# Optimization experiments

Hardware: AMD Instinct MI355X
Metric: run time of the kernel (lower is better)

The kernel has to match this reference:

```python
import jax, jax.numpy as jnp
import numpy as np

B, T, C = 2, 2048, 1024
N_HEAD = 16
HEAD_DIM = C // N_HEAD  # 64


def _apply_rope(x, inv_freq):
    # x: [B, H, T, hd]. Matches the torch module's mixed RoPE variant:
    # cos/sin built from cat(freqs, freqs) but x split by even/odd strides.
    Tn, hd = x.shape[2], x.shape[3]
    t = jnp.arange(Tn, dtype=inv_freq.dtype)
    freqs = t[:, None] * inv_freq[None, :]            # [T, hd/2]
    emb = jnp.concatenate([freqs, freqs], axis=-1)    # [T, hd]
    cos = jnp.cos(emb)[None, None, :, :]
    sin = jnp.sin(emb)[None, None, :, :]
    x1 = x[..., 0::2]
    x2 = x[..., 1::2]
    # interleave (-x2, x1) back to last dim: stack then flatten last two dims
    x_rot = jnp.stack((-x2, x1), axis=-1).reshape(x.shape)
    return x * cos + x_rot * sin


def setup_inputs() -> dict:
    key = jax.random.key(0)
    k1, k2, k3 = jax.random.split(key, 3)
    x = jax.random.normal(k1, (B, T, C), dtype=jnp.float32)
    w_qkv = jax.random.normal(k2, (C, 3 * C), dtype=jnp.float32) * 0.02
    w_proj = jax.random.normal(k3, (C, C), dtype=jnp.float32) * 0.02
    return {"x": x, "w_qkv": w_qkv, "w_proj": w_proj}


def reference(x, w_qkv, w_proj):
    Bn, Tn, Cn = x.shape
    hd = HEAD_DIM
    inv_freq = 1.0 / (10000.0 ** (jnp.arange(0, hd, 2, dtype=jnp.float32) / hd))

    qkv = jnp.einsum('btc,cd->btd', x, w_qkv)  # [B, T, 3C]
    q, k, v = jnp.split(qkv, 3, axis=2)
    # [B, T, C] -> [B, H, T, hd]
    q = q.reshape(Bn, Tn, N_HEAD, hd).transpose(0, 2, 1, 3)
    k = k.reshape(Bn, Tn, N_HEAD, hd).transpose(0, 2, 1, 3)
    v = v.reshape(Bn, Tn, N_HEAD, hd).transpose(0, 2, 1, 3)

    q = _apply_rope(q, inv_freq)
    k = _apply_rope(k, inv_freq)

    scale = 1.0 / jnp.sqrt(jnp.asarray(hd, dtype=q.dtype))
    scores = jnp.einsum('bhqd,bhkd->bhqk', q, k) * scale  # [B, H, T, T]
    causal = jnp.tril(jnp.ones((Tn, Tn), dtype=bool))
    scores = jnp.where(causal[None, None, :, :], scores, -jnp.inf)
    attn = jax.nn.softmax(scores, axis=-1)
    out = jnp.einsum('bhqk,bhkd->bhqd', attn, v)          # [B, H, T, hd]
    y = out.transpose(0, 2, 1, 3).reshape(Bn, Tn, Cn)     # [B, T, C]
    return jnp.einsum('btc,cd->btd', y, w_proj)
```

## Files before the change

### kernel.cpp

```cpp
#include <hip/hip_runtime.h>
#include <hip/hip_bf16.h>

typedef unsigned short u16;
typedef unsigned int u32;
typedef __attribute__((ext_vector_type(8))) __bf16 bf16x8;
typedef __attribute__((ext_vector_type(4))) float f32x4;
typedef __attribute__((ext_vector_type(4))) u16 u16x4;
typedef __attribute__((ext_vector_type(4))) u32 u32x4;

__device__ __forceinline__ u16 f2bf(float f) {
  return __builtin_bit_cast(u16, (__bf16)f);
}
__device__ __forceinline__ float bf2f(u16 h) {
  return __builtin_bit_cast(float, (u32)h << 16);
}

__device__ __forceinline__ void gload_lds16(const void* g, void* l) {
  __builtin_amdgcn_global_load_lds((const __attribute__((address_space(1))) void*)g,
                                   (__attribute__((address_space(3))) void*)l, 16, 0, 0);
}

__global__ __launch_bounds__(256) void cvt_kernel(const float* __restrict__ in, u16* __restrict__ out) {
  const int i = (blockIdx.x * 256 + threadIdx.x) * 4;
  const float4 v = *(const float4*)(in + i);
  u16x4 r = {f2bf(v.x), f2bf(v.y), f2bf(v.z), f2bf(v.w)};
  *(u16x4*)(out + i) = r;
}

__global__ __launch_bounds__(256) void transpose_w(const float* __restrict__ w, u16* __restrict__ wt,
                                                   int K, int N) {
  __shared__ u16 tile[64][65];
  const int n0 = blockIdx.x * 64, k0 = blockIdx.y * 64;
  const int tid = threadIdx.x;
#pragma unroll
  for (int it = 0; it < 16; ++it) {
    const int idx = it * 256 + tid;
    const int r = idx >> 6, c = idx & 63;
    tile[r][c] = f2bf(w[(size_t)(k0 + r) * N + n0 + c]);
  }
  __syncthreads();
#pragma unroll
  for (int it = 0; it < 16; ++it) {
    const int idx = it * 256 + tid;
    const int r2 = idx >> 6, c2 = idx & 63;
    wt[(size_t)(n0 + r2) * K + k0 + c2] = tile[c2][r2];
  }
}

template <int OUT_F32>
__global__ __launch_bounds__(256) void gemm_bt(const u16* __restrict__ A, const u16* __restrict__ Bt,
                                               void* __restrict__ Cout, int M, int N, int K) {
  __shared__ u16 As[2][128 * 32];
  __shared__ u16 Bs[2][128 * 32];
  const int tid = threadIdx.x;
  const int wave = tid >> 6;
  const int lane = tid & 63;
  const int la = lane & 15, lb = lane >> 4;
  const int nwg = gridDim.x * gridDim.y;
  int lid = blockIdx.y * gridDim.x + blockIdx.x;
  lid = (lid & 7) * (nwg >> 3) + (lid >> 3);
  const int m0 = (lid % gridDim.x) * 128, n0 = (lid / gridDim.x) * 128;
  const int wr = (wave >> 1) * 64, wc = (wave & 1) * 64;
  const int srow = lane >> 2;
  const int scol = (lane & 3) * 8;
  const int c0 = wave * 2;

  auto stage = [&](int bb, int k0) {
#pragma unroll
    for (int c2 = 0; c2 < 2; ++c2) {
      const int c = c0 + c2;
      const int row = c * 16 + srow;
      gload_lds16(A + (size_t)(m0 + row) * K + k0 + scol, As[bb] + c * 512);
      gload_lds16(Bt + (size_t)(n0 + row) * K + k0 + scol, Bs[bb] + c * 512);
    }
  };

  f32x4 acc[4][4] = {};
  const int nk = K >> 5;
  stage(0, 0);
  __syncthreads();
  int cur = 0;
  for (int t = 0; t < nk; ++t) {
    if (t + 1 < nk) stage(cur ^ 1, (t + 1) * 32);
    bf16x8 af[4], bfr[4];
#pragma unroll
    for (int m = 0; m < 4; ++m) af[m] = *(const bf16x8*)&As[cur][(wr + m * 16 + la) * 32 + lb * 8];
#pragma unroll
    for (int n = 0; n < 4; ++n) bfr[n] = *(const bf16x8*)&Bs[cur][(wc + n * 16 + la) * 32 + lb * 8];
#pragma unroll
    for (int m = 0; m < 4; ++m)
#pragma unroll
      for (int n = 0; n < 4; ++n)
        acc[m][n] = __builtin_amdgcn_mfma_f32_16x16x32_bf16(af[m], bfr[n], acc[m][n], 0, 0, 0);
    __syncthreads();
    cur ^= 1;
  }
#pragma unroll
  for (int m = 0; m < 4; ++m)
#pragma unroll
    for (int n = 0; n < 4; ++n)
#pragma unroll
      for (int j = 0; j < 4; ++j) {
        const int row = m0 + wr + m * 16 + lb * 4 + j;
        const int col = n0 + wc + n * 16 + la;
        if (OUT_F32)
          ((float*)Cout)[(size_t)row * N + col] = acc[m][n][j];
        else
          ((u16*)Cout)[(size_t)row * N + col] = f2bf(acc[m][n][j]);
      }
}

__global__ __launch_bounds__(256) void rope_kernel(const u16* __restrict__ QKV, u16* __restrict__ Q,
                                                   u16* __restrict__ K, u16* __restrict__ Vt) {
  const int tt = blockIdx.x * 64;
  const int bh = blockIdx.y;
  const int b = bh >> 4, h = bh & 15;
  const int tid = threadIdx.x;
  __shared__ u16 vtile[64][65];
  const float NEG = -0.41524101186f;
  const float QSC = 0.18033688011f;

  const int i = tid & 31;
  const int d0 = 2 * i;
  const int j0 = d0 & 31, j1 = (d0 + 1) & 31;
  const float invf0 = exp2f(NEG * (float)j0);
  const float invf1 = exp2f(NEG * (float)j1);
  const int tl0 = tid >> 5;
  float s0, c0v, s1, c1v, sd0, cd0, sd1, cd1;
  sincosf((float)(tt + tl0) * invf0, &s0, &c0v);
  sincosf((float)(tt + tl0) * invf1, &s1, &c1v);
  sincosf(8.0f * invf0, &sd0, &cd0);
  sincosf(8.0f * invf1, &sd1, &cd1);

#pragma unroll
  for (int it = 0; it < 8; ++it) {
    const int t = tt + tl0 + it * 8;
    const size_t base = ((size_t)(b * 2048 + t)) * 3072 + h * 64 + d0;
    const size_t ob = ((size_t)bh * 2048 + t) * 64 + d0;
    {
      const float x0 = bf2f(QKV[base]), x1 = bf2f(QKV[base + 1]);
      const u32 lo = f2bf((x0 * c0v - x1 * s0) * QSC);
      const u32 hi = f2bf((x1 * c1v + x0 * s1) * QSC);
      *(u32*)(Q + ob) = lo | (hi << 16);
    }
    {
      const float x0 = bf2f(QKV[base + 1024]), x1 = bf2f(QKV[base + 1025]);
      const u32 lo = f2bf(x0 * c0v - x1 * s0);
      const u32 hi = f2bf(x1 * c1v + x0 * s1);
      *(u32*)(K + ob) = lo | (hi << 16);
    }
    const float nc0 = c0v * cd0 - s0 * sd0, ns0 = s0 * cd0 + c0v * sd0;
    c0v = nc0; s0 = ns0;
    const float nc1 = c1v * cd1 - s1 * sd1, ns1 = s1 * cd1 + c1v * sd1;
    c1v = nc1; s1 = ns1;
  }
#pragma unroll
  for (int it = 0; it < 8; ++it) {
    const int idx = it * 256 + tid;
    const int tl = idx >> 5, dd = (idx & 31) * 2;
    const size_t base = ((size_t)(b * 2048 + tt + tl)) * 3072 + 2048 + h * 64 + dd;
    vtile[tl][dd] = QKV[base];
    vtile[tl][dd + 1] = QKV[base + 1];
  }
  __syncthreads();
#pragma unroll
  for (int it = 0; it < 8; ++it) {
    const int idx = it * 256 + tid;
    const int dl = idx >> 5, tp = (idx & 31) * 2;
    const u32 val = (u32)vtile[tp][dl] | ((u32)vtile[tp + 1][dl] << 16);
    *(u32*)(Vt + ((size_t)bh * 64 + dl) * 2048 + tt + tp) = val;
  }
}

__global__ __launch_bounds__(256) void attn_kernel(const u16* __restrict__ Q, const u16* __restrict__ K,
                                                   const u16* __restrict__ Vt, u16* __restrict__ Y) {
  const int L = blockIdx.y * 16 + blockIdx.x;
  const int xcd = L & 7, slot = L >> 3;
  const int bh = xcd * 4 + (slot & 3);
  const int B0 = slot >> 2;
  const int b = bh >> 4, h = bh & 15;
  const int wave = threadIdx.x >> 6, lane = threadIdx.x & 63;
  const int la = lane & 15, lb = lane >> 4;
  const int NT = 32 - B0;
  const int ktE0 = B0 + 1;
  const int q0s[2] = {B0 * 64 + wave * 16, (31 - B0) * 64 + wave * 16};

  __shared__ __align__(16) u16 KV[2][2][4096];

  const size_t plane = (size_t)bh * (2048 * 64);
  const char* Kb = (const char*)(K + plane);
  const char* Vb = (const char*)(Vt + plane);

  auto stage = [&](int buf, int kt) {
#pragma unroll
    for (int it = 0; it < 2; ++it) {
      const int ci = it * 256 + wave * 64 + lane;
      const int row = ci >> 3;
      const int cbs = ((ci & 7) * 16) ^ ((row & 7) << 4);
      const int n2 = row >> 4, rho = row & 15;
      const int srow = ((n2 & 1) << 5) + ((rho >> 2) << 3) + ((n2 >> 1) << 2) + (rho & 3);
      gload_lds16(Kb + (size_t)(kt * 64 + srow) * 128 + cbs,
                  (char*)&KV[buf][0][0] + it * 4096 + wave * 1024);
      gload_lds16(Vb + (size_t)row * 4096 + (size_t)kt * 128 + cbs,
                  (char*)&KV[buf][1][0] + it * 4096 + wave * 1024);
    }
  };

  stage(0, 0);

  bf16x8 qf[2][2];
#pragma unroll
  for (int st = 0; st < 2; ++st)
#pragma unroll
    for (int s = 0; s < 2; ++s)
      qf[st][s] = *(const bf16x8*)(Q + plane + (size_t)(q0s[st] + la) * 64 + s * 32 + lb * 8);

  f32x4 o[2][4] = {};
  float mreg[2] = {-1.0e30f, -1.0e30f};
  float plr[2] = {0.f, 0.f};

  const int x0 = (la & 7) << 4;
  const int cu0 = ((lb * 16) ^ x0) >> 1;
  const int cu1 = ((64 + lb * 16) ^ x0) >> 1;

  __syncthreads();
  int buf = 0;
  for (int kt = 0; kt < NT; ++kt) {
    if (kt + 1 < NT) stage(buf ^ 1, kt + 1);
    const u16* Kc = KV[buf][0];
    const u16* Vc = KV[buf][1];

    bf16x8 kf[2][4];
#pragma unroll
    for (int n = 0; n < 4; ++n) {
      kf[0][n] = *(const bf16x8*)&Kc[(n * 16 + la) * 64 + cu0];
      kf[1][n] = *(const bf16x8*)&Kc[(n * 16 + la) * 64 + cu1];
    }

    bf16x8 paf[2][2];

#pragma unroll
    for (int st = 0; st < 2; ++st) {
      if (st == 0 && kt >= ktE0) continue;
      const int q0 = q0s[st];
      const int rowq = q0 + la;
      f32x4 sa[4] = {};
      __builtin_amdgcn_s_setprio(1);
#pragma unroll
      for (int s = 0; s < 2; ++s)
#pragma unroll
        for (int n = 0; n < 4; ++n)
          sa[n] = __builtin_amdgcn_mfma_f32_16x16x32_bf16(kf[s][n], qf[st][s], sa[n], 0, 0, 0);
      __builtin_amdgcn_s_setprio(0);
      if (kt * 64 + 63 > q0) {
#pragma unroll
        for (int n = 0; n < 4; ++n)
#pragma unroll
          for (int j = 0; j < 4; ++j) {
            const int col = kt * 64 + ((n & 1) << 5) + (lb << 3) + ((n >> 1) << 2) + j;
            if (col > rowq) sa[n][j] = -1.0e30f;
          }
      }
      float lmax = -1.0e30f;
#pragma unroll
      for (int n = 0; n < 4; ++n)
#pragma unroll
        for (int j = 0; j < 4; ++j) lmax = fmaxf(lmax, sa[n][j]);
      if (__any(lmax > mreg[st] + 8.0f)) {
        float v = fmaxf(lmax, __shfl_xor(lmax, 16));
        v = fmaxf(v, __shfl_xor(v, 32));
        const float mn = fmaxf(mreg[st], v);
        const float al = __builtin_amdgcn_exp2f(mreg[st] - mn);
        plr[st] *= al;
        mreg[st] = mn;
        float alj[4];
#pragma unroll
        for (int j = 0; j < 4; ++j) alj[j] = __shfl(al, lb * 4 + j);
#pragma unroll
        for (int n = 0; n < 4; ++n)
#pragma unroll
          for (int j = 0; j < 4; ++j) o[st][n][j] *= alj[j];
      }
      u32 w[4][2];
      float ps = 0.f;
#pragma unroll
      for (int n = 0; n < 4; ++n) {
        const float p0 = __builtin_amdgcn_exp2f(sa[n][0] - mreg[st]);
        const float p1 = __builtin_amdgcn_exp2f(sa[n][1] - mreg[st]);
        const float p2 = __builtin_amdgcn_exp2f(sa[n][2] - mreg[st]);
        const float p3 = __builtin_amdgcn_exp2f(sa[n][3] - mreg[st]);
        ps += (p0 + p1) + (p2 + p3);
        w[n][0] = (u32)f2bf(p0) | ((u32)f2bf(p1) << 16);
        w[n][1] = (u32)f2bf(p2) | ((u32)f2bf(p3) << 16);
      }
      plr[st] += ps;
      paf[st][0] = __builtin_bit_cast(bf16x8, (u32x4){w[0][0], w[0][1], w[2][0], w[2][1]});
      paf[st][1] = __builtin_bit_cast(bf16x8, (u32x4){w[1][0], w[1][1], w[3][0], w[3][1]});
    }

    bf16x8 vf[2][4];
#pragma unroll
    for (int n = 0; n < 4; ++n) {
      vf[0][n] = *(const bf16x8*)&Vc[(n * 16 + la) * 64 + cu0];
      vf[1][n] = *(const bf16x8*)&Vc[(n * 16 + la) * 64 + cu1];
    }
#pragma unroll
    for (int st = 0; st < 2; ++st) {
      if (st == 0 && kt >= ktE0) continue;
      __builtin_amdgcn_s_setprio(1);
#pragma unroll
      for (int n = 0; n < 4; ++n)
#pragma unroll
        for (int s = 0; s < 2; ++s)
          o[st][n] = __builtin_amdgcn_mfma_f32_16x16x32_bf16(paf[st][s], vf[s][n], o[st][n], 0, 0, 0);
      __builtin_amdgcn_s_setprio(0);
    }

    __syncthreads();
    buf ^= 1;
  }

#pragma unroll
  for (int st = 0; st < 2; ++st) {
    float ls = plr[st];
    ls += __shfl_xor(ls, 16);
    ls += __shfl_xor(ls, 32);
    const float rinv = __builtin_amdgcn_rcpf(ls);
    float rj[4];
#pragma unroll
    for (int j = 0; j < 4; ++j) rj[j] = __shfl(rinv, lb * 4 + j);
#pragma unroll
    for (int n = 0; n < 4; ++n)
#pragma unroll
      for (int j = 0; j < 4; ++j) {
        const int t = q0s[st] + lb * 4 + j;
        const int c = h * 64 + n * 16 + la;
        Y[((size_t)b * 2048 + t) * 1024 + c] = f2bf(o[st][n][j] * rj[j]);
      }
  }
}

extern "C" void kernel_launch(void* const* d_in, const int* in_sizes, int n_in, void* d_out,
                              int out_size, void* d_ws, size_t ws_size, hipStream_t stream) {
  (void)in_sizes; (void)n_in; (void)out_size; (void)ws_size;
  const float* x = (const float*)d_in[0];
  const float* w_qkv = (const float*)d_in[1];
  const float* w_proj = (const float*)d_in[2];
  char* ws = (char*)d_ws;
  u16* xb     = (u16*)(ws);
  u16* wqkvT  = (u16*)(ws + 8388608);
  u16* wprojT = (u16*)(ws + 14680064);
  u16* qkv    = (u16*)(ws + 16777216);
  u16* q      = (u16*)(ws + 41943040);
  u16* k      = (u16*)(ws + 50331648);
  u16* vt     = (u16*)(ws + 58720256);
  u16* y      = xb;

  cvt_kernel<<<dim3(4096), dim3(256), 0, stream>>>(x, xb);
  transpose_w<<<dim3(48, 16), dim3(256), 0, stream>>>(w_qkv, wqkvT, 1024, 3072);
  transpose_w<<<dim3(16, 16), dim3(256), 0, stream>>>(w_proj, wprojT, 1024, 1024);
  gemm_bt<0><<<dim3(32, 24), dim3(256), 0, stream>>>(xb, wqkvT, (void*)qkv, 4096, 3072, 1024);
  rope_kernel<<<dim3(32, 32), dim3(256), 0, stream>>>(qkv, q, k, vt);
  attn_kernel<<<dim3(16, 32), dim3(256), 0, stream>>>(q, k, vt, y);
  gemm_bt<1><<<dim3(32, 8), dim3(256), 0, stream>>>(y, wprojT, d_out, 4096, 1024, 1024);
}
```

Before: 119.9 us.

## Split paired causal query tiles into one tile per block, largest first

The attention kernel previously had each block handle two query tiles, B0 and 31-B0, which shared K/V staging and balanced causal work per block. Now each block handles a single 64-row query tile, the grid doubles to 1024 blocks, and the heaviest tiles are scheduled first so the GPU's queue balances the load. This cuts registers per thread and raises parallelism, which may improve occupancy. In exchange, K/V tiles are staged from memory about twice as often in total, since tiles are no longer shared between two query tiles.

```diff
diff --git a/kernel.cpp b/kernel.cpp
--- a/kernel.cpp
+++ b/kernel.cpp
@@ -174,16 +174,15 @@
 
 __global__ __launch_bounds__(256) void attn_kernel(const u16* __restrict__ Q, const u16* __restrict__ K,
                                                    const u16* __restrict__ Vt, u16* __restrict__ Y) {
-  const int L = blockIdx.y * 16 + blockIdx.x;
+  const int L = blockIdx.y * 32 + blockIdx.x;
   const int xcd = L & 7, slot = L >> 3;
   const int bh = xcd * 4 + (slot & 3);
-  const int B0 = slot >> 2;
+  const int beta = 31 - (slot >> 2);
   const int b = bh >> 4, h = bh & 15;
   const int wave = threadIdx.x >> 6, lane = threadIdx.x & 63;
   const int la = lane & 15, lb = lane >> 4;
-  const int NT = 32 - B0;
-  const int ktE0 = B0 + 1;
-  const int q0s[2] = {B0 * 64 + wave * 16, (31 - B0) * 64 + wave * 16};
+  const int q0 = beta * 64 + wave * 16;
+  const int NT = beta + 1;
 
   __shared__ __align__(16) u16 KV[2][2][4096];
 
@@ -208,16 +207,14 @@
 
   stage(0, 0);
 
-  bf16x8 qf[2][2];
-#pragma unroll
-  for (int st = 0; st < 2; ++st)
-#pragma unroll
-    for (int s = 0; s < 2; ++s)
-      qf[st][s] = *(const bf16x8*)(Q + plane + (size_t)(q0s[st] + la) * 64 + s * 32 + lb * 8);
-
-  f32x4 o[2][4] = {};
-  float mreg[2] = {-1.0e30f, -1.0e30f};
-  float plr[2] = {0.f, 0.f};
+  bf16x8 qf[2];
+#pragma unroll
+  for (int s = 0; s < 2; ++s)
+    qf[s] = *(const bf16x8*)(Q + plane + (size_t)(q0 + la) * 64 + s * 32 + lb * 8);
+
+  f32x4 o[4] = {};
+  float mreg = -1.0e30f;
+  float plr = 0.f;
 
   const int x0 = (la & 7) << 4;
   const int cu0 = ((lb * 16) ^ x0) >> 1;
@@ -237,66 +234,60 @@
       kf[1][n] = *(const bf16x8*)&Kc[(n * 16 + la) * 64 + cu1];
     }
 
-    bf16x8 paf[2][2];
-
-#pragma unroll
-    for (int st = 0; st < 2; ++st) {
-      if (st == 0 && kt >= ktE0) continue;
-      const int q0 = q0s[st];
-      const int rowq = q0 + la;
-      f32x4 sa[4] = {};
-      __builtin_amdgcn_s_setprio(1);
-#pragma unroll
-      for (int s = 0; s < 2; ++s)
-#pragma unroll
-        for (int n = 0; n < 4; ++n)
-          sa[n] = __builtin_amdgcn_mfma_f32_16x16x32_bf16(kf[s][n], qf[st][s], sa[n], 0, 0, 0);
-      __builtin_amdgcn_s_setprio(0);
-      if (kt * 64 + 63 > q0) {
-#pragma unroll
-        for (int n = 0; n < 4; ++n)
-#pragma unroll
-          for (int j = 0; j < 4; ++j) {
-            const int col = kt * 64 + ((n & 1) << 5) + (lb << 3) + ((n >> 1) << 2) + j;
-            if (col > rowq) sa[n][j] = -1.0e30f;
-          }
-      }
-      float lmax = -1.0e30f;
+    const int rowq = q0 + la;
+    f32x4 sa[4] = {};
+    __builtin_amdgcn_s_setprio(1);
+#pragma unroll
+    for (int s = 0; s < 2; ++s)
 #pragma unroll
       for (int n = 0; n < 4; ++n)
-#pragma unroll
-        for (int j = 0; j < 4; ++j) lmax = fmaxf(lmax, sa[n][j]);
-      if (__any(lmax > mreg[st] + 8.0f)) {
-        float v = fmaxf(lmax, __shfl_xor(lmax, 16));
-        v = fmaxf(v, __shfl_xor(v, 32));
-        const float mn = fmaxf(mreg[st], v);
-        const float al = __builtin_amdgcn_exp2f(mreg[st] - mn);
-        plr[st] *= al;
-        mreg[st] = mn;
-        float alj[4];
-#pragma unroll
-        for (int j = 0; j < 4; ++j) alj[j] = __shfl(al, lb * 4 + j);
-#pragma unroll
-        for (int n = 0; n < 4; ++n)
-#pragma unroll
-          for (int j = 0; j < 4; ++j) o[st][n][j] *= alj[j];
-      }
-      u32 w[4][2];
-      float ps = 0.f;
-#pragma unroll
-      for (int n = 0; n < 4; ++n) {
-        const float p0 = __builtin_amdgcn_exp2f(sa[n][0] - mreg[st]);
-        const float p1 = __builtin_amdgcn_exp2f(sa[n][1] - mreg[st]);
-        const float p2 = __builtin_amdgcn_exp2f(sa[n][2] - mreg[st]);
-        const float p3 = __builtin_amdgcn_exp2f(sa[n][3] - mreg[st]);
-        ps += (p0 + p1) + (p2 + p3);
-        w[n][0] = (u32)f2bf(p0) | ((u32)f2bf(p1) << 16);
-        w[n][1] = (u32)f2bf(p2) | ((u32)f2bf(p3) << 16);
-      }
-      plr[st] += ps;
-      paf[st][0] = __builtin_bit_cast(bf16x8, (u32x4){w[0][0], w[0][1], w[2][0], w[2][1]});
-      paf[st][1] = __builtin_bit_cast(bf16x8, (u32x4){w[1][0], w[1][1], w[3][0], w[3][1]});
-    }
+        sa[n] = __builtin_amdgcn_mfma_f32_16x16x32_bf16(kf[s][n], qf[s], sa[n], 0, 0, 0);
+    __builtin_amdgcn_s_setprio(0);
+    if (kt == NT - 1) {
+#pragma unroll
+      for (int n = 0; n < 4; ++n)
+#pragma unroll
+        for (int j = 0; j < 4; ++j) {
+          const int col = kt * 64 + ((n & 1) << 5) + (lb << 3) + ((n >> 1) << 2) + j;
+          if (col > rowq) sa[n][j] = -1.0e30f;
+        }
+    }
+    float mn_[4];
+#pragma unroll
+    for (int n = 0; n < 4; ++n)
+      mn_[n] = fmaxf(fmaxf(sa[n][0], sa[n][1]), fmaxf(sa[n][2], sa[n][3]));
+    const float lmax = fmaxf(fmaxf(mn_[0], mn_[1]), fmaxf(mn_[2], mn_[3]));
+    if (__any(lmax > mreg + 8.0f)) {
+      float v = fmaxf(lmax, __shfl_xor(lmax, 16));
+      v = fmaxf(v, __shfl_xor(v, 32));
+      const float mn = fmaxf(mreg, v);
+      const float al = __builtin_amdgcn_exp2f(mreg - mn);
+      plr *= al;
+      mreg = mn;
+      float alj[4];
+#pragma unroll
+      for (int j = 0; j < 4; ++j) alj[j] = __shfl(al, lb * 4 + j);
+#pragma unroll
+      for (int n = 0; n < 4; ++n)
+#pragma unroll
+        for (int j = 0; j < 4; ++j) o[n][j] *= alj[j];
+    }
+    u32 w[4][2];
+    float ps = 0.f;
+#pragma unroll
+    for (int n = 0; n < 4; ++n) {
+      const float p0 = __builtin_amdgcn_exp2f(sa[n][0] - mreg);
+      const float p1 = __builtin_amdgcn_exp2f(sa[n][1] - mreg);
+      const float p2 = __builtin_amdgcn_exp2f(sa[n][2] - mreg);
+      const float p3 = __builtin_amdgcn_exp2f(sa[n][3] - mreg);
+      ps += (p0 + p1) + (p2 + p3);
+      w[n][0] = (u32)f2bf(p0) | ((u32)f2bf(p1) << 16);
+      w[n][1] = (u32)f2bf(p2) | ((u32)f2bf(p3) << 16);
+    }
+    plr += ps;
+    bf16x8 paf[2];
+    paf[0] = __builtin_bit_cast(bf16x8, (u32x4){w[0][0], w[0][1], w[2][0], w[2][1]});
+    paf[1] = __builtin_bit_cast(bf16x8, (u32x4){w[1][0], w[1][1], w[3][0], w[3][1]});
 
     bf16x8 vf[2][4];
 #pragma unroll
@@ -304,40 +295,33 @@
       vf[0][n] = *(const bf16x8*)&Vc[(n * 16 + la) * 64 + cu0];
       vf[1][n] = *(const bf16x8*)&Vc[(n * 16 + la) * 64 + cu1];
     }
-#pragma unroll
-    for (int st = 0; st < 2; ++st) {
-      if (st == 0 && kt >= ktE0) continue;
-      __builtin_amdgcn_s_setprio(1);
-#pragma unroll
-      for (int n = 0; n < 4; ++n)
-#pragma unroll
-        for (int s = 0; s < 2; ++s)
-          o[st][n] = __builtin_amdgcn_mfma_f32_16x16x32_bf16(paf[st][s], vf[s][n], o[st][n], 0, 0, 0);
-      __builtin_amdgcn_s_setprio(0);
-    }
+    __builtin_amdgcn_s_setprio(1);
+#pragma unroll
+    for (int n = 0; n < 4; ++n)
+#pragma unroll
+      for (int s = 0; s < 2; ++s)
+        o[n] = __builtin_amdgcn_mfma_f32_16x16x32_bf16(paf[s], vf[s][n], o[n], 0, 0, 0);
+    __builtin_amdgcn_s_setprio(0);
 
     __syncthreads();
     buf ^= 1;
   }
 
-#pragma unroll
-  for (int st = 0; st < 2; ++st) {
-    float ls = plr[st];
-    ls += __shfl_xor(ls, 16);
-    ls += __shfl_xor(ls, 32);
-    const float rinv = __builtin_amdgcn_rcpf(ls);
-    float rj[4];
-#pragma unroll
-    for (int j = 0; j < 4; ++j) rj[j] = __shfl(rinv, lb * 4 + j);
-#pragma unroll
-    for (int n = 0; n < 4; ++n)
-#pragma unroll
-      for (int j = 0; j < 4; ++j) {
-        const int t = q0s[st] + lb * 4 + j;
-        const int c = h * 64 + n * 16 + la;
-        Y[((size_t)b * 2048 + t) * 1024 + c] = f2bf(o[st][n][j] * rj[j]);
-      }
-  }
+  float ls = plr;
+  ls += __shfl_xor(ls, 16);
+  ls += __shfl_xor(ls, 32);
+  const float rinv = __builtin_amdgcn_rcpf(ls);
+  float rj[4];
+#pragma unroll
+  for (int j = 0; j < 4; ++j) rj[j] = __shfl(rinv, lb * 4 + j);
+#pragma unroll
+  for (int n = 0; n < 4; ++n)
+#pragma unroll
+    for (int j = 0; j < 4; ++j) {
+      const int t = q0 + lb * 4 + j;
+      const int c = h * 64 + n * 16 + la;
+      Y[((size_t)b * 2048 + t) * 1024 + c] = f2bf(o[n][j] * rj[j]);
+    }
 }
 
 extern "C" void kernel_launch(void* const* d_in, const int* in_sizes, int n_in, void* d_out,
@@ -361,6 +345,6 @@
   transpose_w<<<dim3(16, 16), dim3(256), 0, stream>>>(w_proj, wprojT, 1024, 1024);
   gemm_bt<0><<<dim3(32, 24), dim3(256), 0, stream>>>(xb, wqkvT, (void*)qkv, 4096, 3072, 1024);
   rope_kernel<<<dim3(32, 32), dim3(256), 0, stream>>>(qkv, q, k, vt);
-  attn_kernel<<<dim3(16, 32), dim3(256), 0, stream>>>(q, k, vt, y);
+  attn_kernel<<<dim3(32, 32), dim3(256), 0, stream>>>(q, k, vt, y);
   gemm_bt<1><<<dim3(32, 8), dim3(256), 0, stream>>>(y, wprojT, d_out, 4096, 1024, 1024);
 }
```

After: 119.9 us. Within noise of the previous version (+0.0%).
